# Kernel tuning notes

Measured on AMD Instinct MI355X. Metric: run time of the kernel, lower is better.

## Reference

```python
import jax, jax.numpy as jnp
import numpy as np

INV_TEMP = 10.0

def pairwise_distance(x, y):
    # squared L2 distance: [b,n,c],[b,m,c] -> [b,n,m]
    x2 = jnp.sum(x * x, axis=-1, keepdims=True)          # [b,n,1]
    y2 = jnp.sum(y * y, axis=-1)[:, None, :]             # [b,1,m]
    xy = jnp.einsum('bnc,bmc->bnm', x, y)                # [b,n,m]
    return x2 + y2 - 2.0 * xy

def setup_inputs() -> dict:
    key = jax.random.key(0)
    k1, k2, k3 = jax.random.split(key, 3)
    b, n, m, c = 4, 4096, 4096, 32
    x_f = jax.random.normal(k1, (b, n, c), dtype=jnp.float32)
    y_f = jax.random.normal(k2, (b, m, c), dtype=jnp.float32)
    y_c = jax.random.normal(k3, (b, m, 3), dtype=jnp.float32)
    temp_inv = jnp.ones((1,), dtype=jnp.float32) * INV_TEMP
    return {"x_f": x_f, "y_f": y_f, "y_c": y_c, "temp_inv": temp_inv}

def reference(x_f, y_f, y_c, temp_inv):
    # corr_type='soft', st=True (straight-through)
    dist = pairwise_distance(x_f, y_f)                   # [b,n,m]
    y_soft = jax.nn.softmax(-dist * temp_inv[0], axis=2) # [b,n,m]
    index = jnp.argmax(y_soft, axis=2)                   # [b,n]
    y_hard = jax.nn.one_hot(index, y_soft.shape[2], dtype=y_soft.dtype)
    ret = y_hard - jax.lax.stop_gradient(y_soft) + y_soft
    x_corr = jnp.matmul(ret, y_c)                        # [b,n,3]
    return x_corr
```

## Files before the change

### kernel.cpp

```cpp
#include <hip/hip_runtime.h>

#define B 4
#define N 4096
#define M 4096
#define C 32
#define BN (B * N)

typedef short bf16x8 __attribute__((ext_vector_type(8)));
typedef float f32x4  __attribute__((ext_vector_type(4)));
typedef unsigned int u32x4 __attribute__((ext_vector_type(4)));

__device__ __forceinline__ float bf16lo(unsigned int u) { return __uint_as_float(u << 16); }
__device__ __forceinline__ float bf16hi(unsigned int u) { return __uint_as_float(u & 0xffff0000u); }

__device__ __forceinline__ void split3(const float f[8], bf16x8& h, bf16x8& m, bf16x8& l) {
    u32x4 hw, mw, lw;
    #pragma unroll
    for (int p = 0; p < 4; ++p) {
        const float f0 = f[2*p], f1 = f[2*p+1];
        const unsigned int h0 = __float_as_uint(f0) & 0xffff0000u;
        const unsigned int h1 = __float_as_uint(f1) & 0xffff0000u;
        hw[p] = h1 | (h0 >> 16);
        const float r0 = f0 - __uint_as_float(h0);
        const float r1 = f1 - __uint_as_float(h1);
        const unsigned int m0 = __float_as_uint(r0) & 0xffff0000u;
        const unsigned int m1 = __float_as_uint(r1) & 0xffff0000u;
        mw[p] = m1 | (m0 >> 16);
        const float s0 = r0 - __uint_as_float(m0);
        const float s1 = r1 - __uint_as_float(m1);
        lw[p] = (__float_as_uint(s1) & 0xffff0000u) | (__float_as_uint(s0) >> 16);
    }
    h = __builtin_bit_cast(bf16x8, hw);
    m = __builtin_bit_cast(bf16x8, mw);
    l = __builtin_bit_cast(bf16x8, lw);
}

__global__ __launch_bounds__(256, 2)
void nn_main(const void* __restrict__ xptr, const void* __restrict__ yptr,
             const unsigned short* __restrict__ tptr,
             float* __restrict__ wD, int* __restrict__ wI) {
    const bool is_bf16 = (tptr[0] == 0x4120);

    __shared__ float y2s[512];

    const int tid  = threadIdx.x;
    const int lane = tid & 63;
    const int bi   = blockIdx.x;

    const int wv   = tid >> 6;
    const int col  = lane & 15;
    const int quad = lane >> 4;
    const int ms   = bi & 7;
    const int nb   = (bi >> 3) & 15;
    const int b    = bi >> 7;
    const int n_base = nb * 256 + wv * 64;

    float bD[4][4];
    int   bI[4][4];
    #pragma unroll
    for (int t = 0; t < 4; ++t)
        #pragma unroll
        for (int r = 0; r < 4; ++r) { bD[t][r] = -__builtin_inff(); bI[t][r] = 0; }

    if (is_bf16) {
        const unsigned short* yp = (const unsigned short*)yptr;
        const unsigned short* xp = (const unsigned short*)xptr;

        for (int r = tid; r < 512; r += 256) {
            const int m = ms * 512 + r;
            const uint4* p = (const uint4*)(yp + ((size_t)b * M + m) * C);
            float s = 0.f;
            #pragma unroll
            for (int i = 0; i < 4; ++i) {
                uint4 v = p[i];
                float f;
                f = bf16lo(v.x); s = fmaf(f, f, s); f = bf16hi(v.x); s = fmaf(f, f, s);
                f = bf16lo(v.y); s = fmaf(f, f, s); f = bf16hi(v.y); s = fmaf(f, f, s);
                f = bf16lo(v.z); s = fmaf(f, f, s); f = bf16hi(v.z); s = fmaf(f, f, s);
                f = bf16lo(v.w); s = fmaf(f, f, s); f = bf16hi(v.w); s = fmaf(f, f, s);
            }
            y2s[r] = -0.5f * s;
        }

        bf16x8 af[4];
        #pragma unroll
        for (int t = 0; t < 4; ++t)
            af[t] = *(const bf16x8*)(xp + ((size_t)b * N + n_base + t * 16 + col) * C + quad * 8);

        __syncthreads();

        const unsigned short* yb = yp + ((size_t)b * M + ms * 512) * C;

        bf16x8 bfr = *(const bf16x8*)(yb + (size_t)col * C + quad * 8);
        for (int mt = 0; mt < 32; ++mt) {
            bf16x8 bnx = bfr;
            if (mt < 31)
                bnx = *(const bf16x8*)(yb + (size_t)((mt + 1) * 16 + col) * C + quad * 8);
            const float y2c  = y2s[mt * 16 + col];
            const int   mcur = ms * 512 + mt * 16 + col;
            #pragma unroll
            for (int t = 0; t < 4; ++t) {
                f32x4 acc = {y2c, y2c, y2c, y2c};
                acc = __builtin_amdgcn_mfma_f32_16x16x32_bf16(af[t], bfr, acc, 0, 0, 0);
                #pragma unroll
                for (int r = 0; r < 4; ++r) {
                    if (acc[r] > bD[t][r]) { bD[t][r] = acc[r]; bI[t][r] = mcur; }
                }
            }
            bfr = bnx;
        }
    } else {
        const float* yp = (const float*)yptr;
        const float* xp = (const float*)xptr;

        for (int r = tid; r < 512; r += 256) {
            const float* p = yp + ((size_t)b * M + ms * 512 + r) * C;
            float s = 0.f;
            #pragma unroll
            for (int i = 0; i < 8; ++i) {
                float4 v = *(const float4*)(p + i * 4);
                s = fmaf(v.x, v.x, s); s = fmaf(v.y, v.y, s);
                s = fmaf(v.z, v.z, s); s = fmaf(v.w, v.w, s);
            }
            y2s[r] = -0.5f * s;
        }

        bf16x8 ah[4], am[4], al[4];
        #pragma unroll
        for (int t = 0; t < 4; ++t) {
            const float* xr = xp + ((size_t)b * N + n_base + t * 16 + col) * C + quad * 8;
            float4 v0 = *(const float4*)xr;
            float4 v1 = *(const float4*)(xr + 4);
            const float xf[8] = {v0.x, v0.y, v0.z, v0.w, v1.x, v1.y, v1.z, v1.w};
            split3(xf, ah[t], am[t], al[t]);
        }

        __syncthreads();

        const float* yb = yp + ((size_t)b * M + ms * 512) * C;

        const float* y0 = yb + (size_t)col * C + quad * 8;
        float4 c0 = *(const float4*)y0;
        float4 c1 = *(const float4*)(y0 + 4);

        for (int mt = 0; mt < 32; ++mt) {
            float4 n0 = c0, n1 = c1;
            if (mt < 31) {
                const float* nr = yb + (size_t)((mt + 1) * 16 + col) * C + quad * 8;
                n0 = *(const float4*)nr;
                n1 = *(const float4*)(nr + 4);
            }
            const float cf[8] = {c0.x, c0.y, c0.z, c0.w, c1.x, c1.y, c1.z, c1.w};
            bf16x8 bh, bm, bl;
            split3(cf, bh, bm, bl);

            const float y2c  = y2s[mt * 16 + col];
            const int   mcur = ms * 512 + mt * 16 + col;
            #pragma unroll
            for (int t = 0; t < 4; ++t) {
                f32x4 acc = {y2c, y2c, y2c, y2c};
                acc = __builtin_amdgcn_mfma_f32_16x16x32_bf16(ah[t], bh, acc, 0, 0, 0);
                acc = __builtin_amdgcn_mfma_f32_16x16x32_bf16(am[t], bh, acc, 0, 0, 0);
                acc = __builtin_amdgcn_mfma_f32_16x16x32_bf16(al[t], bh, acc, 0, 0, 0);
                acc = __builtin_amdgcn_mfma_f32_16x16x32_bf16(ah[t], bm, acc, 0, 0, 0);
                acc = __builtin_amdgcn_mfma_f32_16x16x32_bf16(am[t], bm, acc, 0, 0, 0);
                acc = __builtin_amdgcn_mfma_f32_16x16x32_bf16(al[t], bm, acc, 0, 0, 0);
                acc = __builtin_amdgcn_mfma_f32_16x16x32_bf16(ah[t], bl, acc, 0, 0, 0);
                acc = __builtin_amdgcn_mfma_f32_16x16x32_bf16(am[t], bl, acc, 0, 0, 0);
                acc = __builtin_amdgcn_mfma_f32_16x16x32_bf16(al[t], bl, acc, 0, 0, 0);
                #pragma unroll
                for (int r = 0; r < 4; ++r) {
                    if (acc[r] > bD[t][r]) { bD[t][r] = acc[r]; bI[t][r] = mcur; }
                }
            }
            c0 = n0; c1 = n1;
        }
    }

    #pragma unroll
    for (int mask = 1; mask < 16; mask <<= 1) {
        #pragma unroll
        for (int t = 0; t < 4; ++t)
            #pragma unroll
            for (int r = 0; r < 4; ++r) {
                float oD = __shfl_xor(bD[t][r], mask, 64);
                int   oI = __shfl_xor(bI[t][r], mask, 64);
                if (oD > bD[t][r] || (oD == bD[t][r] && oI < bI[t][r])) {
                    bD[t][r] = oD; bI[t][r] = oI;
                }
            }
    }

    if (col == 0) {
        #pragma unroll
        for (int t = 0; t < 4; ++t)
            #pragma unroll
            for (int r = 0; r < 4; ++r) {
                const int n = n_base + t * 16 + quad * 4 + r;
                const size_t g = (size_t)ms * BN + (size_t)b * N + n;
                wD[g] = bD[t][r];
                wI[g] = bI[t][r];
            }
    }
}

__global__ __launch_bounds__(256)
void nn_combine(const float* __restrict__ wD, const int* __restrict__ wI,
                const void* __restrict__ ycptr,
                const unsigned short* __restrict__ tptr,
                void* __restrict__ outptr) {
    const bool is_bf16 = (tptr[0] == 0x4120);
    const int i = blockIdx.x * 256 + threadIdx.x;
    if (i >= BN) return;
    const int b = i >> 12;

    float bk = wD[i];
    int   bx = wI[i];
    #pragma unroll
    for (int s = 1; s < 8; ++s) {
        const float k  = wD[(size_t)s * BN + i];
        const int   ix = wI[(size_t)s * BN + i];
        if (k > bk || (k == bk && ix < bx)) { bk = k; bx = ix; }
    }

    const size_t src = ((size_t)b * M + bx) * 3;
    if (is_bf16) {
        const unsigned short* yc = (const unsigned short*)ycptr;
        unsigned short* o = (unsigned short*)outptr;
        o[i*3+0] = yc[src+0];
        o[i*3+1] = yc[src+1];
        o[i*3+2] = yc[src+2];
    } else {
        const float* yc = (const float*)ycptr;
        float* o = (float*)outptr;
        o[i*3+0] = yc[src+0];
        o[i*3+1] = yc[src+1];
        o[i*3+2] = yc[src+2];
    }
}

extern "C" void kernel_launch(void* const* d_in, const int* in_sizes, int n_in,
                              void* d_out, int out_size, void* d_ws, size_t ws_size,
                              hipStream_t stream) {
    const void* x  = d_in[0];
    const void* y  = d_in[1];
    const void* yc = d_in[2];
    const unsigned short* t = (const unsigned short*)d_in[3];

    float* wD = (float*)d_ws;
    int*   wI = (int*)((char*)d_ws + (size_t)8 * BN * sizeof(float));

    nn_main<<<512, 256, 0, stream>>>(x, y, t, wD, wI);
    nn_combine<<<(BN + 255) / 256, 256, 0, stream>>>(wD, wI, yc, t, d_out);
}
```

Measured before the change: 104.0 us.

## Precompute y bf16 split and norms in prepass, halve per-wave rows, shuffle combine

Adds a prepass kernel that splits y into three bf16 parts and computes the squared norms once, so the main kernel no longer repeats that split for every n-block. The main kernel now gives each wave 32 rows instead of 64 and launches twice as many blocks with a higher occupancy hint. The combine step now reduces the 8 partial argmax slices with wave shuffles. The trade-off is an extra launch, extra workspace traffic for the three bf16 copies, and less reuse of each loaded y tile per wave.

Measured after the change: 96.22 us. 1.08x faster.

```diff
diff --git a/kernel.cpp b/kernel.cpp
--- a/kernel.cpp
+++ b/kernel.cpp
@@ -9,6 +9,12 @@
 typedef short bf16x8 __attribute__((ext_vector_type(8)));
 typedef float f32x4  __attribute__((ext_vector_type(4)));
 typedef unsigned int u32x4 __attribute__((ext_vector_type(4)));
+
+#define WS_WI ((size_t)8 * BN * 4)
+#define WS_YH (WS_WI * 2)
+#define WS_YM (WS_YH + (size_t)B * M * C * 2)
+#define WS_YL (WS_YM + (size_t)B * M * C * 2)
+#define WS_Y2 (WS_YL + (size_t)B * M * C * 2)
 
 __device__ __forceinline__ float bf16lo(unsigned int u) { return __uint_as_float(u << 16); }
 __device__ __forceinline__ float bf16hi(unsigned int u) { return __uint_as_float(u & 0xffff0000u); }
@@ -35,32 +41,66 @@
     l = __builtin_bit_cast(bf16x8, lw);
 }
 
-__global__ __launch_bounds__(256, 2)
+__global__ __launch_bounds__(256)
+void y_prepass(const void* __restrict__ yptr, const unsigned short* __restrict__ tptr,
+               void* __restrict__ ws) {
+    if (tptr[0] == 0x4120) return;
+    unsigned short* yh = (unsigned short*)((char*)ws + WS_YH);
+    unsigned short* ym = (unsigned short*)((char*)ws + WS_YM);
+    unsigned short* yl = (unsigned short*)((char*)ws + WS_YL);
+    float*          y2 = (float*)((char*)ws + WS_Y2);
+
+    const int gid = blockIdx.x * 256 + threadIdx.x;
+    const int row = gid >> 2;
+    const int seg = gid & 3;
+    const float* p = (const float*)yptr + (size_t)row * C + seg * 8;
+    float4 v0 = *(const float4*)p;
+    float4 v1 = *(const float4*)(p + 4);
+    const float f[8] = {v0.x, v0.y, v0.z, v0.w, v1.x, v1.y, v1.z, v1.w};
+
+    bf16x8 h, m, l;
+    split3(f, h, m, l);
+    const size_t o = (size_t)row * C + seg * 8;
+    *(bf16x8*)(yh + o) = h;
+    *(bf16x8*)(ym + o) = m;
+    *(bf16x8*)(yl + o) = l;
+
+    float s = 0.f;
+    #pragma unroll
+    for (int k = 0; k < 8; ++k) s = fmaf(f[k], f[k], s);
+    s += __shfl_xor(s, 1, 64);
+    s += __shfl_xor(s, 2, 64);
+    if (seg == 0) y2[row] = -0.5f * s;
+}
+
+__global__ __launch_bounds__(256, 4)
 void nn_main(const void* __restrict__ xptr, const void* __restrict__ yptr,
-             const unsigned short* __restrict__ tptr,
-             float* __restrict__ wD, int* __restrict__ wI) {
+             const unsigned short* __restrict__ tptr, void* __restrict__ ws) {
+    float* wD = (float*)ws;
+    int*   wI = (int*)((char*)ws + WS_WI);
     const bool is_bf16 = (tptr[0] == 0x4120);
 
     __shared__ float y2s[512];
 
     const int tid  = threadIdx.x;
     const int lane = tid & 63;
-    const int bi   = blockIdx.x;
-
     const int wv   = tid >> 6;
     const int col  = lane & 15;
     const int quad = lane >> 4;
+    const int bi   = blockIdx.x;
     const int ms   = bi & 7;
-    const int nb   = (bi >> 3) & 15;
-    const int b    = bi >> 7;
-    const int n_base = nb * 256 + wv * 64;
-
-    float bD[4][4];
-    int   bI[4][4];
-    #pragma unroll
-    for (int t = 0; t < 4; ++t)
+    const int nb   = (bi >> 3) & 31;
+    const int b    = bi >> 8;
+    const int n_base = nb * 128 + wv * 32;
+
+    float bD[2][4];
+    int   bI[2][4];
+    #pragma unroll
+    for (int t = 0; t < 2; ++t)
         #pragma unroll
         for (int r = 0; r < 4; ++r) { bD[t][r] = -__builtin_inff(); bI[t][r] = 0; }
+
+    const size_t boff = (size_t)col * C + quad * 8;
 
     if (is_bf16) {
         const unsigned short* yp = (const unsigned short*)yptr;
@@ -82,52 +122,42 @@
             y2s[r] = -0.5f * s;
         }
 
-        bf16x8 af[4];
-        #pragma unroll
-        for (int t = 0; t < 4; ++t)
+        bf16x8 af[2];
+        #pragma unroll
+        for (int t = 0; t < 2; ++t)
             af[t] = *(const bf16x8*)(xp + ((size_t)b * N + n_base + t * 16 + col) * C + quad * 8);
 
         __syncthreads();
 
         const unsigned short* yb = yp + ((size_t)b * M + ms * 512) * C;
-
-        bf16x8 bfr = *(const bf16x8*)(yb + (size_t)col * C + quad * 8);
+        bf16x8 bfr = *(const bf16x8*)(yb + boff);
         for (int mt = 0; mt < 32; ++mt) {
             bf16x8 bnx = bfr;
-            if (mt < 31)
-                bnx = *(const bf16x8*)(yb + (size_t)((mt + 1) * 16 + col) * C + quad * 8);
+            if (mt < 31) bnx = *(const bf16x8*)(yb + boff + (size_t)(mt + 1) * (16 * C));
             const float y2c  = y2s[mt * 16 + col];
             const int   mcur = ms * 512 + mt * 16 + col;
             #pragma unroll
-            for (int t = 0; t < 4; ++t) {
+            for (int t = 0; t < 2; ++t) {
                 f32x4 acc = {y2c, y2c, y2c, y2c};
                 acc = __builtin_amdgcn_mfma_f32_16x16x32_bf16(af[t], bfr, acc, 0, 0, 0);
                 #pragma unroll
-                for (int r = 0; r < 4; ++r) {
+                for (int r = 0; r < 4; ++r)
                     if (acc[r] > bD[t][r]) { bD[t][r] = acc[r]; bI[t][r] = mcur; }
-                }
             }
             bfr = bnx;
         }
     } else {
-        const float* yp = (const float*)yptr;
+        const unsigned short* yh = (const unsigned short*)((char*)ws + WS_YH) + ((size_t)b * M + ms * 512) * C;
+        const unsigned short* ym = (const unsigned short*)((char*)ws + WS_YM) + ((size_t)b * M + ms * 512) * C;
+        const unsigned short* yl = (const unsigned short*)((char*)ws + WS_YL) + ((size_t)b * M + ms * 512) * C;
+        const float*         y2g = (const float*)((char*)ws + WS_Y2) + (size_t)b * M + ms * 512;
+
+        for (int r = tid; r < 512; r += 256) y2s[r] = y2g[r];
+
         const float* xp = (const float*)xptr;
-
-        for (int r = tid; r < 512; r += 256) {
-            const float* p = yp + ((size_t)b * M + ms * 512 + r) * C;
-            float s = 0.f;
-            #pragma unroll
-            for (int i = 0; i < 8; ++i) {
-                float4 v = *(const float4*)(p + i * 4);
-                s = fmaf(v.x, v.x, s); s = fmaf(v.y, v.y, s);
-                s = fmaf(v.z, v.z, s); s = fmaf(v.w, v.w, s);
-            }
-            y2s[r] = -0.5f * s;
-        }
-
-        bf16x8 ah[4], am[4], al[4];
-        #pragma unroll
-        for (int t = 0; t < 4; ++t) {
+        bf16x8 ah[2], am[2], al[2];
+        #pragma unroll
+        for (int t = 0; t < 2; ++t) {
             const float* xr = xp + ((size_t)b * N + n_base + t * 16 + col) * C + quad * 8;
             float4 v0 = *(const float4*)xr;
             float4 v1 = *(const float4*)(xr + 4);
@@ -137,50 +167,43 @@
 
         __syncthreads();
 
-        const float* yb = yp + ((size_t)b * M + ms * 512) * C;
-
-        const float* y0 = yb + (size_t)col * C + quad * 8;
-        float4 c0 = *(const float4*)y0;
-        float4 c1 = *(const float4*)(y0 + 4);
-
+        bf16x8 bh = *(const bf16x8*)(yh + boff);
+        bf16x8 bmi = *(const bf16x8*)(ym + boff);
+        bf16x8 bl = *(const bf16x8*)(yl + boff);
         for (int mt = 0; mt < 32; ++mt) {
-            float4 n0 = c0, n1 = c1;
+            bf16x8 nh = bh, nm = bmi, nl = bl;
             if (mt < 31) {
-                const float* nr = yb + (size_t)((mt + 1) * 16 + col) * C + quad * 8;
-                n0 = *(const float4*)nr;
-                n1 = *(const float4*)(nr + 4);
-            }
-            const float cf[8] = {c0.x, c0.y, c0.z, c0.w, c1.x, c1.y, c1.z, c1.w};
-            bf16x8 bh, bm, bl;
-            split3(cf, bh, bm, bl);
-
+                const size_t no = boff + (size_t)(mt + 1) * (16 * C);
+                nh = *(const bf16x8*)(yh + no);
+                nm = *(const bf16x8*)(ym + no);
+                nl = *(const bf16x8*)(yl + no);
+            }
             const float y2c  = y2s[mt * 16 + col];
             const int   mcur = ms * 512 + mt * 16 + col;
             #pragma unroll
-            for (int t = 0; t < 4; ++t) {
+            for (int t = 0; t < 2; ++t) {
                 f32x4 acc = {y2c, y2c, y2c, y2c};
-                acc = __builtin_amdgcn_mfma_f32_16x16x32_bf16(ah[t], bh, acc, 0, 0, 0);
-                acc = __builtin_amdgcn_mfma_f32_16x16x32_bf16(am[t], bh, acc, 0, 0, 0);
-                acc = __builtin_amdgcn_mfma_f32_16x16x32_bf16(al[t], bh, acc, 0, 0, 0);
-                acc = __builtin_amdgcn_mfma_f32_16x16x32_bf16(ah[t], bm, acc, 0, 0, 0);
-                acc = __builtin_amdgcn_mfma_f32_16x16x32_bf16(am[t], bm, acc, 0, 0, 0);
-                acc = __builtin_amdgcn_mfma_f32_16x16x32_bf16(al[t], bm, acc, 0, 0, 0);
-                acc = __builtin_amdgcn_mfma_f32_16x16x32_bf16(ah[t], bl, acc, 0, 0, 0);
-                acc = __builtin_amdgcn_mfma_f32_16x16x32_bf16(am[t], bl, acc, 0, 0, 0);
-                acc = __builtin_amdgcn_mfma_f32_16x16x32_bf16(al[t], bl, acc, 0, 0, 0);
+                acc = __builtin_amdgcn_mfma_f32_16x16x32_bf16(ah[t], bh,  acc, 0, 0, 0);
+                acc = __builtin_amdgcn_mfma_f32_16x16x32_bf16(am[t], bh,  acc, 0, 0, 0);
+                acc = __builtin_amdgcn_mfma_f32_16x16x32_bf16(al[t], bh,  acc, 0, 0, 0);
+                acc = __builtin_amdgcn_mfma_f32_16x16x32_bf16(ah[t], bmi, acc, 0, 0, 0);
+                acc = __builtin_amdgcn_mfma_f32_16x16x32_bf16(am[t], bmi, acc, 0, 0, 0);
+                acc = __builtin_amdgcn_mfma_f32_16x16x32_bf16(al[t], bmi, acc, 0, 0, 0);
+                acc = __builtin_amdgcn_mfma_f32_16x16x32_bf16(ah[t], bl,  acc, 0, 0, 0);
+                acc = __builtin_amdgcn_mfma_f32_16x16x32_bf16(am[t], bl,  acc, 0, 0, 0);
+                acc = __builtin_amdgcn_mfma_f32_16x16x32_bf16(al[t], bl,  acc, 0, 0, 0);
                 #pragma unroll
-                for (int r = 0; r < 4; ++r) {
+                for (int r = 0; r < 4; ++r)
                     if (acc[r] > bD[t][r]) { bD[t][r] = acc[r]; bI[t][r] = mcur; }
-                }
-            }
-            c0 = n0; c1 = n1;
+            }
+            bh = nh; bmi = nm; bl = nl;
         }
     }
 
     #pragma unroll
     for (int mask = 1; mask < 16; mask <<= 1) {
         #pragma unroll
-        for (int t = 0; t < 4; ++t)
+        for (int t = 0; t < 2; ++t)
             #pragma unroll
             for (int r = 0; r < 4; ++r) {
                 float oD = __shfl_xor(bD[t][r], mask, 64);
@@ -193,7 +216,7 @@
 
     if (col == 0) {
         #pragma unroll
-        for (int t = 0; t < 4; ++t)
+        for (int t = 0; t < 2; ++t)
             #pragma unroll
             for (int r = 0; r < 4; ++r) {
                 const int n = n_base + t * 16 + quad * 4 + r;
@@ -210,32 +233,38 @@
                 const unsigned short* __restrict__ tptr,
                 void* __restrict__ outptr) {
     const bool is_bf16 = (tptr[0] == 0x4120);
-    const int i = blockIdx.x * 256 + threadIdx.x;
-    if (i >= BN) return;
-    const int b = i >> 12;
-
-    float bk = wD[i];
-    int   bx = wI[i];
-    #pragma unroll
-    for (int s = 1; s < 8; ++s) {
-        const float k  = wD[(size_t)s * BN + i];
-        const int   ix = wI[(size_t)s * BN + i];
-        if (k > bk || (k == bk && ix < bx)) { bk = k; bx = ix; }
-    }
-
-    const size_t src = ((size_t)b * M + bx) * 3;
-    if (is_bf16) {
-        const unsigned short* yc = (const unsigned short*)ycptr;
-        unsigned short* o = (unsigned short*)outptr;
-        o[i*3+0] = yc[src+0];
-        o[i*3+1] = yc[src+1];
-        o[i*3+2] = yc[src+2];
-    } else {
-        const float* yc = (const float*)ycptr;
-        float* o = (float*)outptr;
-        o[i*3+0] = yc[src+0];
-        o[i*3+1] = yc[src+1];
-        o[i*3+2] = yc[src+2];
+    const int tid  = threadIdx.x;
+    const int lane = tid & 63;
+    const int wv   = tid >> 6;
+    const int s    = lane >> 3;
+    const int ro   = lane & 7;
+    const int row  = blockIdx.x * 32 + wv * 8 + ro;
+
+    float k  = wD[(size_t)s * BN + row];
+    int   ix = wI[(size_t)s * BN + row];
+    #pragma unroll
+    for (int mask = 8; mask < 64; mask <<= 1) {
+        float ok = __shfl_xor(k, mask, 64);
+        int   oi = __shfl_xor(ix, mask, 64);
+        if (ok > k || (ok == k && oi < ix)) { k = ok; ix = oi; }
+    }
+
+    if (s == 0) {
+        const int b = row >> 12;
+        const size_t src = ((size_t)b * M + ix) * 3;
+        if (is_bf16) {
+            const unsigned short* yc = (const unsigned short*)ycptr;
+            unsigned short* o = (unsigned short*)outptr;
+            o[row*3+0] = yc[src+0];
+            o[row*3+1] = yc[src+1];
+            o[row*3+2] = yc[src+2];
+        } else {
+            const float* yc = (const float*)ycptr;
+            float* o = (float*)outptr;
+            o[row*3+0] = yc[src+0];
+            o[row*3+1] = yc[src+1];
+            o[row*3+2] = yc[src+2];
+        }
     }
 }
 
@@ -248,8 +277,9 @@
     const unsigned short* t = (const unsigned short*)d_in[3];
 
     float* wD = (float*)d_ws;
-    int*   wI = (int*)((char*)d_ws + (size_t)8 * BN * sizeof(float));
-
-    nn_main<<<512, 256, 0, stream>>>(x, y, t, wD, wI);
-    nn_combine<<<(BN + 255) / 256, 256, 0, stream>>>(wD, wI, yc, t, d_out);
-}
+    int*   wI = (int*)((char*)d_ws + WS_WI);
+
+    y_prepass<<<256, 256, 0, stream>>>(y, t, d_ws);
+    nn_main<<<1024, 256, 0, stream>>>(x, y, t, d_ws);
+    nn_combine<<<512, 256, 0, stream>>>(wD, wI, yc, t, d_out);
+}
```
